# Kernel tuning notes

Measured on AMD Instinct MI355X. Metric: run time of the kernel, lower is better.

Reference implementation:

```python
import jax, jax.numpy as jnp
import numpy as np

B = 16384
F = 128   # num_features
H = 128   # hidden_dim
E = 32    # embedding_dim


def setup_inputs() -> dict:
    key = jax.random.key(0)
    k_x, k_w1, k_b1, k_w2, k_b2 = jax.random.split(key, 5)
    # Per-feature params stacked along feature axis.
    # Layer 1: Linear(1 -> H): weight [F, H] (in_dim==1 squeezed), bias [F, H]
    # Layer 2: Linear(H -> E): weight [F, H, E], bias [F, E]
    # Torch default init: U(-1/sqrt(fan_in), 1/sqrt(fan_in))
    w1 = jax.random.uniform(k_w1, (F, H), jnp.float32, -1.0, 1.0)          # fan_in=1
    b1 = jax.random.uniform(k_b1, (F, H), jnp.float32, -1.0, 1.0)
    bound2 = 1.0 / np.sqrt(H)
    w2 = jax.random.uniform(k_w2, (F, H, E), jnp.float32, -bound2, bound2)
    b2 = jax.random.uniform(k_b2, (F, E), jnp.float32, -bound2, bound2)
    x = jax.random.normal(k_x, (B, F), jnp.float32)
    return {"x": x, "w1": w1, "b1": b1, "w2": w2, "b2": b2}


def reference(x, w1, b1, w2, b2):
    # Fused over features: broadcast-mul replaces K=1 matmuls,
    # single batched GEMM replaces per-feature second Linear.
    h = jax.nn.relu(x[:, :, None] * w1[None] + b1[None])   # [B, F, H]
    out = jnp.einsum('bfh,fhe->bfe', h, w2) + b2[None]      # [B, F, E]
    return out.reshape(x.shape[0], F * E)                   # concat along last dim
```

## Files before the change

### kernel.cpp

```cpp
#include <hip/hip_runtime.h>
#include <math.h>

#define B_N 16384
#define F_N 128
#define H_N 128
#define E_N 32
#define ROWS (H_N + 1)

typedef float f4v __attribute__((ext_vector_type(4)));

__device__ __forceinline__ int eidxA(int e) { return ((e >> 2) << 3) | (e & 3); }

__global__ __launch_bounds__(128) void build_tables(
    const float* __restrict__ w1, const float* __restrict__ b1,
    const float* __restrict__ w2, const float* __restrict__ b2,
    float* __restrict__ ts_out, float* __restrict__ tab)
{
    __shared__ float w1s[H_N], b1s[H_N], ts[H_N];
    __shared__ int   hidx[H_N];
    __shared__ float w2s[H_N * E_N];
    __shared__ float dA[H_N * E_N];
    __shared__ float dC[H_N * E_N];
    __shared__ float baseA[4 * E_N], baseC[4 * E_N];
    __shared__ float gtA[4 * E_N], gtC[4 * E_N];

    const int f   = blockIdx.x;
    const int tid = threadIdx.x;

    float w1v = w1[f * H_N + tid];
    float b1v = b1[f * H_N + tid];
    w1s[tid] = w1v;
    b1s[tid] = b1v;
    ts[tid]   = (w1v != 0.0f) ? (-b1v / w1v) : INFINITY;
    hidx[tid] = tid;

    {
        const float4* src = (const float4*)(w2 + (size_t)f * H_N * E_N);
        float4*       dst = (float4*)w2s;
        #pragma unroll
        for (int it = 0; it < 8; ++it) dst[it * 128 + tid] = src[it * 128 + tid];
    }
    __syncthreads();

    for (int k = 2; k <= H_N; k <<= 1) {
        for (int j = k >> 1; j > 0; j >>= 1) {
            int ixj = tid ^ j;
            if (ixj > tid) {
                float a = ts[tid], bv = ts[ixj];
                bool up = ((tid & k) == 0);
                bool sw = up ? (a > bv) : (a < bv);
                if (sw) {
                    int ia = hidx[tid];
                    ts[tid] = bv; ts[ixj] = a;
                    hidx[tid] = hidx[ixj]; hidx[ixj] = ia;
                }
            }
            __syncthreads();
        }
    }

    ts_out[f * H_N + tid] = ts[tid];

    const int e = tid & 31;
    const int g = tid >> 5;

    #pragma unroll 4
    for (int jj = 0; jj < 32; ++jj) {
        int   j   = g * 32 + jj;
        int   p   = hidx[j];
        float w1h = w1s[p], b1h = b1s[p];
        float w2v = w2s[p * E_N + e];
        float s   = (w1h > 0.f) ? 1.f : ((w1h < 0.f) ? -1.f : 0.f);
        dA[j * E_N + e] = s * w1h * w2v;
        dC[j * E_N + e] = s * b1h * w2v;
    }
    {
        float pA = 0.f, pC = 0.f;
        #pragma unroll 4
        for (int hh = 0; hh < 32; ++hh) {
            int   h   = g * 32 + hh;
            float w1h = w1s[h], b1h = b1s[h];
            float w2v = w2s[h * E_N + e];
            if (w1h < 0.f) {
                pA = fmaf(w1h, w2v, pA);
                pC = fmaf(b1h, w2v, pC);
            } else if (w1h == 0.f && b1h > 0.f) {
                pC = fmaf(b1h, w2v, pC);
            }
        }
        baseA[g * E_N + e] = pA;
        baseC[g * E_N + e] = pC;
    }

    {
        float aA = 0.f, aC = 0.f;
        for (int jj = 0; jj < 32; ++jj) {
            int idx = (g * 32 + jj) * E_N + e;
            aA += dA[idx]; dA[idx] = aA;
            aC += dC[idx]; dC[idx] = aC;
        }
        gtA[g * E_N + e] = aA;
        gtC[g * E_N + e] = aC;
    }
    __syncthreads();

    float offA = baseA[e] + baseA[E_N + e] + baseA[2 * E_N + e] + baseA[3 * E_N + e];
    float offC = baseC[e] + baseC[E_N + e] + baseC[2 * E_N + e] + baseC[3 * E_N + e]
               + b2[f * E_N + e];
    for (int gg = 0; gg < g; ++gg) {
        offA += gtA[gg * E_N + e];
        offC += gtC[gg * E_N + e];
    }

    const size_t base = (size_t)f * ROWS * 64;
    const int    eA   = eidxA(e);
    if (g == 0) {
        tab[base + eA]     = offA;
        tab[base + eA + 4] = offC;
    }
    #pragma unroll 4
    for (int jj = 0; jj < 32; ++jj) {
        int j = g * 32 + jj;
        tab[base + (size_t)(j + 1) * 64 + eA]     = offA + dA[j * E_N + e];
        tab[base + (size_t)(j + 1) * 64 + eA + 4] = offC + dC[j * E_N + e];
    }
}

#define FH 32
#define NB 32

__global__ __launch_bounds__(256, 8) void apply_tables(
    const float* __restrict__ x, const float* __restrict__ ts,
    const float* __restrict__ tab, float* __restrict__ out)
{
    __shared__ float lds_t[FH * ROWS];

    const int tid = threadIdx.x;

    const unsigned bid  = blockIdx.x;
    const unsigned work = (bid & 7u) * 256u + (bid >> 3);
    const int b0 = (int)(work & 511u) * NB;
    const int f0 = (int)(work >> 9)  * FH;

    {
        const float4* src = (const float4*)(ts + (size_t)f0 * H_N);
        #pragma unroll
        for (int it = 0; it < 4; ++it) {
            int    vi  = it * 256 + tid;
            float4 v   = src[vi];
            int    idx = vi * 4;
            int    fl_ = idx >> 7;
            int    j   = idx & 127;
            float* dst = &lds_t[fl_ * ROWS + j];
            dst[0] = v.x; dst[1] = v.y; dst[2] = v.z; dst[3] = v.w;
        }
    }
    __syncthreads();

    const int lane = tid & 63;
    const int fl   = tid >> 3;
    const int eq   = tid & 7;

    float xv[4]; int lo4[4];
    {
        const float* tloc = &lds_t[fl * ROWS];
        int hi4[4];
        #pragma unroll
        for (int j = 0; j < 4; ++j) {
            xv[j]  = x[(size_t)(b0 + eq * 4 + j) * F_N + f0 + fl];
            lo4[j] = 0; hi4[j] = H_N;
        }
        #pragma unroll
        for (int s = 0; s < 7; ++s) {
            #pragma unroll
            for (int j = 0; j < 4; ++j) {
                int  mid = (lo4[j] + hi4[j]) >> 1;
                bool lt  = tloc[mid] < xv[j];
                lo4[j] = lt ? mid + 1 : lo4[j];
                hi4[j] = lt ? hi4[j] : mid;
            }
        }
    }

    const float* tb = tab + (size_t)(f0 + fl) * ROWS * 64 + eq * 8;
    float*       op = out + (size_t)b0 * (F_N * E_N) + (size_t)(f0 + fl) * E_N + eq * 4;
    const int gbase = lane & 56;

    for (int c = 0; c < 8; ++c) {
        #pragma unroll
        for (int j = 0; j < 4; ++j) {
            int   r   = c * 4 + j;
            int   lo  = __shfl(lo4[j], gbase | c);
            float xvr = __shfl(xv[j],  gbase | c);
            const float* row = tb + (size_t)lo * 64;
            f4v a  = *(const f4v*)(row);
            f4v cc = *(const f4v*)(row + 4);
            f4v o;
            o.x = fmaf(xvr, a.x, cc.x);
            o.y = fmaf(xvr, a.y, cc.y);
            o.z = fmaf(xvr, a.z, cc.z);
            o.w = fmaf(xvr, a.w, cc.w);
            __builtin_nontemporal_store(o, (f4v*)(op + (size_t)r * (F_N * E_N)));
        }
    }
}

__global__ __launch_bounds__(256) void direct_kernel(
    const float* __restrict__ x, const float* __restrict__ w1,
    const float* __restrict__ b1, const float* __restrict__ w2,
    const float* __restrict__ b2, float* __restrict__ out)
{
    __shared__ float w1s[H_N], b1s[H_N], b2s[E_N];
    __shared__ float w2s[H_N * E_N];
    const int f   = blockIdx.y;
    const int tid = threadIdx.x;
    if (tid < H_N) { w1s[tid] = w1[f * H_N + tid]; b1s[tid] = b1[f * H_N + tid]; }
    for (int i = tid; i < H_N * E_N; i += 256) w2s[i] = w2[(size_t)f * H_N * E_N + i];
    if (tid < E_N) b2s[tid] = b2[f * E_N + tid];
    __syncthreads();

    const int b  = blockIdx.x * 256 + tid;
    float xv = x[(size_t)b * F_N + f];
    float acc[E_N];
    #pragma unroll
    for (int e = 0; e < E_N; ++e) acc[e] = b2s[e];
    for (int h = 0; h < H_N; ++h) {
        float hv = fmaxf(fmaf(xv, w1s[h], b1s[h]), 0.f);
        #pragma unroll
        for (int e = 0; e < E_N; ++e) acc[e] = fmaf(hv, w2s[h * E_N + e], acc[e]);
    }
    float* op = out + (size_t)b * (F_N * E_N) + (size_t)f * E_N;
    #pragma unroll
    for (int e = 0; e < E_N; e += 4)
        *(float4*)(op + e) = make_float4(acc[e], acc[e + 1], acc[e + 2], acc[e + 3]);
}

extern "C" void kernel_launch(void* const* d_in, const int* in_sizes, int n_in,
                              void* d_out, int out_size, void* d_ws, size_t ws_size,
                              hipStream_t stream) {
    const float* x  = (const float*)d_in[0];
    const float* w1 = (const float*)d_in[1];
    const float* b1 = (const float*)d_in[2];
    const float* w2 = (const float*)d_in[3];
    const float* b2 = (const float*)d_in[4];
    float* out = (float*)d_out;

    const size_t n_ts  = (size_t)F_N * H_N;
    const size_t n_tab = (size_t)F_N * ROWS * 64;
    const size_t need  = (n_ts + n_tab) * sizeof(float);

    if (ws_size >= need) {
        float* ts  = (float*)d_ws;
        float* tab = ts + n_ts;
        build_tables<<<dim3(F_N), dim3(128), 0, stream>>>(w1, b1, w2, b2, ts, tab);
        apply_tables<<<dim3((B_N / NB) * (F_N / FH)), dim3(256), 0, stream>>>(x, ts, tab, out);
    } else {
        direct_kernel<<<dim3(B_N / 256, F_N), dim3(256), 0, stream>>>(x, w1, b1, w2, b2, out);
    }
}
```

Measured before the change: 299.6 us.

## Retile apply_tables to 16 features x 64 rows with LDS-staged x and indices

Changes the apply_tables tile from 32 features x 32 batch rows to 16 features x 64 rows. x is now loaded coalesced with float4 into shared memory, and the binary-search results are stored as ushort indices in LDS, replacing the cross-lane shuffles. The block-to-work mapping becomes simpler and launch bounds drop to 6 blocks per CU. The aim is wider coalesced output rows and cheaper index distribution, at the cost of an extra barrier and more LDS use.

Result: no change. 294.4 us (-1.7%).

```diff
diff --git a/kernel.cpp b/kernel.cpp
--- a/kernel.cpp
+++ b/kernel.cpp
@@ -126,26 +126,27 @@
     }
 }
 
-#define FH 32
-#define NB 32
-
-__global__ __launch_bounds__(256, 8) void apply_tables(
+#define FH 16
+#define NB 64
+
+__global__ __launch_bounds__(256, 6) void apply_tables(
     const float* __restrict__ x, const float* __restrict__ ts,
     const float* __restrict__ tab, float* __restrict__ out)
 {
-    __shared__ float lds_t[FH * ROWS];
+    __shared__ float          lds_t[FH * ROWS];
+    __shared__ float          xs[NB * FH];
+    __shared__ unsigned short los[NB * FH];
 
     const int tid = threadIdx.x;
 
-    const unsigned bid  = blockIdx.x;
-    const unsigned work = (bid & 7u) * 256u + (bid >> 3);
-    const int b0 = (int)(work & 511u) * NB;
-    const int f0 = (int)(work >> 9)  * FH;
+    const unsigned bid = blockIdx.x;
+    const int f0 = (int)(bid & 7u) * FH;
+    const int b0 = (int)(bid >> 3) * NB;
 
     {
         const float4* src = (const float4*)(ts + (size_t)f0 * H_N);
         #pragma unroll
-        for (int it = 0; it < 4; ++it) {
+        for (int it = 0; it < 2; ++it) {
             int    vi  = it * 256 + tid;
             float4 v   = src[vi];
             int    idx = vi * 4;
@@ -155,53 +156,62 @@
             dst[0] = v.x; dst[1] = v.y; dst[2] = v.z; dst[3] = v.w;
         }
     }
-    __syncthreads();
-
-    const int lane = tid & 63;
-    const int fl   = tid >> 3;
-    const int eq   = tid & 7;
-
-    float xv[4]; int lo4[4];
-    {
-        const float* tloc = &lds_t[fl * ROWS];
-        int hi4[4];
+    {
+        int bl = tid >> 2;
+        int fq = (tid & 3) * 4;
+        float4 v = *(const float4*)(x + (size_t)(b0 + bl) * F_N + f0 + fq);
+        *(float4*)(&xs[bl * FH + fq]) = v;
+    }
+    __syncthreads();
+
+    {
+        const int fa = tid & 15;
+        const int rg = tid >> 4;
+        const float* tloc = &lds_t[fa * ROWS];
+        float xv[4];
+        int   lo[4], hi[4];
         #pragma unroll
         for (int j = 0; j < 4; ++j) {
-            xv[j]  = x[(size_t)(b0 + eq * 4 + j) * F_N + f0 + fl];
-            lo4[j] = 0; hi4[j] = H_N;
+            xv[j] = xs[(rg * 4 + j) * FH + fa];
+            lo[j] = 0; hi[j] = H_N;
         }
         #pragma unroll
         for (int s = 0; s < 7; ++s) {
             #pragma unroll
             for (int j = 0; j < 4; ++j) {
-                int  mid = (lo4[j] + hi4[j]) >> 1;
+                int  mid = (lo[j] + hi[j]) >> 1;
                 bool lt  = tloc[mid] < xv[j];
-                lo4[j] = lt ? mid + 1 : lo4[j];
-                hi4[j] = lt ? hi4[j] : mid;
+                lo[j] = lt ? mid + 1 : lo[j];
+                hi[j] = lt ? hi[j] : mid;
             }
         }
-    }
-
+        #pragma unroll
+        for (int j = 0; j < 4; ++j)
+            los[(rg * 4 + j) * FH + fa] = (unsigned short)lo[j];
+    }
+    __syncthreads();
+
+    const int fl = (tid >> 3) & 15;
+    const int eq = tid & 7;
+    const int bh = tid >> 7;
+    const int rbase = bh * 32;
     const float* tb = tab + (size_t)(f0 + fl) * ROWS * 64 + eq * 8;
-    float*       op = out + (size_t)b0 * (F_N * E_N) + (size_t)(f0 + fl) * E_N + eq * 4;
-    const int gbase = lane & 56;
-
-    for (int c = 0; c < 8; ++c) {
-        #pragma unroll
-        for (int j = 0; j < 4; ++j) {
-            int   r   = c * 4 + j;
-            int   lo  = __shfl(lo4[j], gbase | c);
-            float xvr = __shfl(xv[j],  gbase | c);
-            const float* row = tb + (size_t)lo * 64;
-            f4v a  = *(const f4v*)(row);
-            f4v cc = *(const f4v*)(row + 4);
-            f4v o;
-            o.x = fmaf(xvr, a.x, cc.x);
-            o.y = fmaf(xvr, a.y, cc.y);
-            o.z = fmaf(xvr, a.z, cc.z);
-            o.w = fmaf(xvr, a.w, cc.w);
-            __builtin_nontemporal_store(o, (f4v*)(op + (size_t)r * (F_N * E_N)));
-        }
+    float*       op = out + (size_t)(b0 + rbase) * (F_N * E_N)
+                          + (size_t)(f0 + fl) * E_N + eq * 4;
+
+    #pragma unroll 4
+    for (int r = 0; r < 32; ++r) {
+        int   lo = los[(rbase + r) * FH + fl];
+        float xv = xs[(rbase + r) * FH + fl];
+        const float* row = tb + (size_t)lo * 64;
+        f4v a  = *(const f4v*)(row);
+        f4v cc = *(const f4v*)(row + 4);
+        f4v o;
+        o.x = fmaf(xv, a.x, cc.x);
+        o.y = fmaf(xv, a.y, cc.y);
+        o.z = fmaf(xv, a.z, cc.z);
+        o.w = fmaf(xv, a.w, cc.w);
+        __builtin_nontemporal_store(o, (f4v*)(op + (size_t)r * (F_N * E_N)));
     }
 }
 
```
